# Kernel tuning notes

Measured on AMD Instinct MI355X. Metric: run time of the kernel, lower is better.

## Reference

```python
import jax, jax.numpy as jnp
import numpy as np

N_NODES = 50000
N_EDGES = 800000
N_GRAPHS = 512
EPS = 1e-5
SLOPE = 0.2  # LeakyReLU negative slope in GATv2


def setup_inputs() -> dict:
    key = jax.random.key(0)
    ks = jax.random.split(key, 20)
    s = 0.1
    inp = {
        "x": jax.random.normal(ks[0], (N_NODES, 9), jnp.float32),
        "edge_attr": jax.random.normal(ks[1], (N_EDGES, 3), jnp.float32),
        "Wl0": jax.random.normal(ks[2], (9, 64), jnp.float32) * s,
        "Wr0": jax.random.normal(ks[3], (9, 64), jnp.float32) * s,
        "bl0": jnp.zeros((64,), jnp.float32),
        "br0": jnp.zeros((64,), jnp.float32),
        "We0": jax.random.normal(ks[4], (3, 64), jnp.float32) * s,
        "att0": jax.random.normal(ks[5], (64,), jnp.float32) * s,
        "bo0": jnp.zeros((64,), jnp.float32),
        "Wl": jax.random.normal(ks[6], (4, 64, 64), jnp.float32) * s,
        "Wr": jax.random.normal(ks[7], (4, 64, 64), jnp.float32) * s,
        "bl": jnp.zeros((4, 64), jnp.float32),
        "br": jnp.zeros((4, 64), jnp.float32),
        "We": jax.random.normal(ks[8], (4, 3, 64), jnp.float32) * s,
        "att": jax.random.normal(ks[9], (4, 64), jnp.float32) * s,
        "bo": jnp.zeros((4, 64), jnp.float32),
        "bn_g": jnp.ones((5, 64), jnp.float32),
        "bn_b": jnp.zeros((5, 64), jnp.float32),
        "bn_m": jnp.zeros((5, 64), jnp.float32),
        "bn_v": jax.random.uniform(ks[10], (5, 64), jnp.float32, 0.5, 1.5),
        "Wjk": jax.random.normal(ks[11], (64, 64), jnp.float32) * s,
        "bjk": jnp.zeros((64,), jnp.float32),
        "Whead": jax.random.normal(ks[12], (64, 1), jnp.float32) * s,
        "bhead": jnp.zeros((1,), jnp.float32),
        "edge_index": jax.random.randint(ks[13], (2, N_EDGES), 0, N_NODES, jnp.int32),
        "batch": jnp.sort(jax.random.randint(ks[14], (N_NODES,), 0, N_GRAPHS, jnp.int32)),
        "num_graphs": N_GRAPHS,
    }
    return inp


def gatv2_layer(h, src, dst, ea, Wl_, bl_, Wr_, br_, We_, a_, bo_, n_nodes):
    # GATv2Conv (heads=1, edge_dim) : e_ij = a . LeakyReLU(Wl h_j + Wr h_i + We e_ij)
    xl = h @ Wl_ + bl_                          # [N, 64] source transform
    xr = h @ Wr_ + br_                          # [N, 64] dest transform
    e = jax.nn.leaky_relu(xl[src] + xr[dst] + ea @ We_, SLOPE)  # [E, 64]
    logit = e @ a_                              # [E]
    m = jax.ops.segment_max(logit, dst, num_segments=n_nodes)
    m = jnp.where(jnp.isfinite(m), m, 0.0)      # empty segments -> -inf
    p = jnp.exp(logit - m[dst])
    z = jax.ops.segment_sum(p, dst, num_segments=n_nodes)
    alpha = p / jnp.maximum(z[dst], 1e-16)      # softmax over in-edges of dst
    out = jax.ops.segment_sum(alpha[:, None] * xl[src], dst, num_segments=n_nodes)
    return out + bo_


def bn_relu(h, g, b, m, v):
    # eval-mode BatchNorm1d followed by ReLU (BasicGNN: norm then act)
    return jax.nn.relu((h - m) * (g * jax.lax.rsqrt(v + EPS)) + b)


def reference(x, edge_attr, Wl0, Wr0, bl0, br0, We0, att0, bo0,
              Wl, Wr, bl, br, We, att, bo,
              bn_g, bn_b, bn_m, bn_v, Wjk, bjk, Whead, bhead,
              edge_index, batch, num_graphs):
    n = x.shape[0]
    src, dst = edge_index[0], edge_index[1]
    h = gatv2_layer(x, src, dst, edge_attr, Wl0, bl0, Wr0, br0, We0, att0, bo0, n)
    h = bn_relu(h, bn_g[0], bn_b[0], bn_m[0], bn_v[0])
    for i in range(4):
        h = gatv2_layer(h, src, dst, edge_attr, Wl[i], bl[i], Wr[i], br[i], We[i], att[i], bo[i], n)
        h = bn_relu(h, bn_g[i + 1], bn_b[i + 1], bn_m[i + 1], bn_v[i + 1])
    h = h @ Wjk + bjk                            # jk='last' output projection 64->64
    # global mean pool over graphs
    sums = jax.ops.segment_sum(h, batch, num_segments=num_graphs)          # [G, 64]
    cnt = jax.ops.segment_sum(jnp.ones((n,), h.dtype), batch, num_segments=num_graphs)
    pooled = sums / jnp.maximum(cnt, 1.0)[:, None]
    return pooled @ Whead + bhead                # [G, 1]  (dropout inactive in eval)
```

## Files before the change

kernel.cpp:

```cpp
#include <hip/hip_runtime.h>
#include <math.h>

#define N_NODES 50000
#define N_EDGES 800000
#define N_GRAPHS 512
#define SLOPE 0.2f
#define CAP 48
static constexpr float EPS_BN = 1e-5f;

typedef float v2f __attribute__((ext_vector_type(2)));


__global__ void scatter_bucket_kernel(const int* __restrict__ src, const int* __restrict__ dst,
                                      const float* __restrict__ ea,
                                      int* __restrict__ cnt,
                                      float4* __restrict__ rec) {
    int e = blockIdx.x * blockDim.x + threadIdx.x;
    if (e < N_EDGES) {
        int d = dst[e];
        int pos = atomicAdd(&cnt[d], 1);
        if (pos < CAP)
            rec[(size_t)d * CAP + pos] = make_float4(__int_as_float(src[e]),
                                                     ea[e * 3 + 0], ea[e * 3 + 1], ea[e * 3 + 2]);
    }
}


__global__ __launch_bounds__(256) void transform9_kernel(
    const float* __restrict__ h,
    const float* __restrict__ Wl, const float* __restrict__ bl,
    const float* __restrict__ Wr, const float* __restrict__ br,
    float* __restrict__ xl, float* __restrict__ xr) {
    int t = threadIdx.x;
    int w = t >> 6;
    int k = t & 63;
    v2f wlr[9];
#pragma unroll
    for (int j = 0; j < 9; j++) wlr[j] = (v2f){Wl[j * 64 + k], Wr[j * 64 + k]};
    v2f bias = {bl[k], br[k]};
    int wid = blockIdx.x * 4 + w;
    const int NW = gridDim.x * 4;
    for (int n = wid; n < N_NODES; n += NW) {
        int un = __builtin_amdgcn_readfirstlane(n);
        const float* __restrict__ hrow = h + (size_t)un * 9;
        float hb[9];
#pragma unroll
        for (int j = 0; j < 9; j++) hb[j] = hrow[j];
        v2f acc = bias;
#pragma unroll
        for (int j = 0; j < 9; j++)
            acc = __builtin_elementwise_fma((v2f){hb[j], hb[j]}, wlr[j], acc);
        xl[(size_t)un * 64 + k] = acc.x;
        xr[(size_t)un * 64 + k] = acc.y;
    }
}


__global__ __launch_bounds__(256) void transform5_kernel(
    const float* __restrict__ h,
    const float* __restrict__ Wl, const float* __restrict__ bl,
    const float* __restrict__ Wr, const float* __restrict__ br,
    float* __restrict__ xl, float* __restrict__ xr) {
    __shared__ float sAt[64][68];
    __shared__ float sB[64][128];
    int t = threadIdx.x;
    int n0 = blockIdx.x * 64;

#pragma unroll
    for (int i = 0; i < 4; i++) {
        int idx = i * 256 + t;
        int row = idx >> 4;
        int fc  = idx & 15;
        int n = n0 + row;
        float4 v = (n < N_NODES) ? *((const float4*)(h + (size_t)n * 64 + fc * 4))
                                 : make_float4(0.f, 0.f, 0.f, 0.f);
        sAt[fc * 4 + 0][row] = v.x;
        sAt[fc * 4 + 1][row] = v.y;
        sAt[fc * 4 + 2][row] = v.z;
        sAt[fc * 4 + 3][row] = v.w;
    }
#pragma unroll
    for (int i = 0; i < 8; i++) {
        int idx = i * 256 + t;
        int j  = idx >> 5;
        int fc = idx & 31;
        int c  = fc * 4;
        float4 v = (c < 64) ? *((const float4*)(Wl + j * 64 + c))
                            : *((const float4*)(Wr + j * 64 + (c - 64)));
        *((float4*)&sB[j][c]) = v;
    }
    __syncthreads();

    int tx = t & 15, ty = t >> 4;
    int col0 = tx * 8;
    const float* bsrc = (col0 < 64) ? (bl + col0) : (br + (col0 - 64));
    v2f acc[4][4];
#pragma unroll
    for (int r = 0; r < 4; r++)
#pragma unroll
        for (int cc = 0; cc < 4; cc++)
            acc[r][cc] = (v2f){bsrc[cc * 2], bsrc[cc * 2 + 1]};

#pragma unroll 4
    for (int j = 0; j < 64; j++) {
        float a0 = sAt[j][ty * 4 + 0];
        float a1 = sAt[j][ty * 4 + 1];
        float a2 = sAt[j][ty * 4 + 2];
        float a3 = sAt[j][ty * 4 + 3];
        float4 bq0 = *((const float4*)&sB[j][col0]);
        float4 bq1 = *((const float4*)&sB[j][col0 + 4]);
        v2f b0 = {bq0.x, bq0.y}, b1 = {bq0.z, bq0.w};
        v2f b2 = {bq1.x, bq1.y}, b3 = {bq1.z, bq1.w};
        v2f a0v = {a0, a0}, a1v = {a1, a1}, a2v = {a2, a2}, a3v = {a3, a3};
        acc[0][0] = __builtin_elementwise_fma(a0v, b0, acc[0][0]);
        acc[0][1] = __builtin_elementwise_fma(a0v, b1, acc[0][1]);
        acc[0][2] = __builtin_elementwise_fma(a0v, b2, acc[0][2]);
        acc[0][3] = __builtin_elementwise_fma(a0v, b3, acc[0][3]);
        acc[1][0] = __builtin_elementwise_fma(a1v, b0, acc[1][0]);
        acc[1][1] = __builtin_elementwise_fma(a1v, b1, acc[1][1]);
        acc[1][2] = __builtin_elementwise_fma(a1v, b2, acc[1][2]);
        acc[1][3] = __builtin_elementwise_fma(a1v, b3, acc[1][3]);
        acc[2][0] = __builtin_elementwise_fma(a2v, b0, acc[2][0]);
        acc[2][1] = __builtin_elementwise_fma(a2v, b1, acc[2][1]);
        acc[2][2] = __builtin_elementwise_fma(a2v, b2, acc[2][2]);
        acc[2][3] = __builtin_elementwise_fma(a2v, b3, acc[2][3]);
        acc[3][0] = __builtin_elementwise_fma(a3v, b0, acc[3][0]);
        acc[3][1] = __builtin_elementwise_fma(a3v, b1, acc[3][1]);
        acc[3][2] = __builtin_elementwise_fma(a3v, b2, acc[3][2]);
        acc[3][3] = __builtin_elementwise_fma(a3v, b3, acc[3][3]);
    }

#pragma unroll
    for (int r = 0; r < 4; r++) {
        int n = n0 + ty * 4 + r;
        if (n < N_NODES) {
            float4 lo = make_float4(acc[r][0].x, acc[r][0].y, acc[r][1].x, acc[r][1].y);
            float4 hi = make_float4(acc[r][2].x, acc[r][2].y, acc[r][3].x, acc[r][3].y);
            float* dst = (col0 < 64) ? (xl + (size_t)n * 64 + col0)
                                     : (xr + (size_t)n * 64 + (col0 - 64));
            *((float4*)dst) = lo;
            *((float4*)(dst + 4)) = hi;
        }
    }
}


__global__ __launch_bounds__(256) void gat_fused4_kernel(
    const float* __restrict__ xl, const float* __restrict__ xr,
    const float4* __restrict__ recP, const int* __restrict__ cnt,
    const float* __restrict__ We, const float* __restrict__ att,
    const float* __restrict__ bo,
    const float* __restrict__ bn_g, const float* __restrict__ bn_b,
    const float* __restrict__ bn_m, const float* __restrict__ bn_v,
    float* __restrict__ hout) {
    int t = threadIdx.x;
    int w = t >> 6;
    int lane = t & 63;
    int q = lane >> 4;
    int r = lane & 15;
    int k4 = r * 4;
    int n = blockIdx.x * 4 + w;

    float4 we0 = *(const float4*)(We + 0 * 64 + k4);
    float4 we1 = *(const float4*)(We + 64 + k4);
    float4 we2 = *(const float4*)(We + 128 + k4);
    float4 at4 = *(const float4*)(att + k4);
    float4 xq  = *(const float4*)(xr + (size_t)n * 64 + k4);
    v2f we0a = {we0.x, we0.y}, we0b = {we0.z, we0.w};
    v2f we1a = {we1.x, we1.y}, we1b = {we1.z, we1.w};
    v2f we2a = {we2.x, we2.y}, we2b = {we2.z, we2.w};
    v2f ata  = {at4.x, at4.y}, atb  = {at4.z, at4.w};
    v2f xra  = {xq.x, xq.y},   xrb  = {xq.z, xq.w};
    int beg = n * CAP;
    int end = beg + min(cnt[n], CAP);

    v2f oAa = {0.f, 0.f}, oAb = {0.f, 0.f};
    v2f oBa = {0.f, 0.f}, oBb = {0.f, 0.f};
    float zA = 0.f, zB = 0.f;

    for (int c = beg; c < end; c += 8) {
        int pA = c + q;     bool vA = pA < end; int iA = vA ? pA : beg;
        int pB = c + 4 + q; bool vB = pB < end; int iB = vB ? pB : beg;
        float4 rA = recP[iA];
        float4 rB = recP[iB];
        int sA = __float_as_int(rA.x);
        int sB = __float_as_int(rB.x);
        float4 xA = *(const float4*)(xl + (size_t)sA * 64 + k4);
        float4 xB = *(const float4*)(xl + (size_t)sB * 64 + k4);
        v2f xAa = {xA.x, xA.y}, xAb = {xA.z, xA.w};
        v2f xBa = {xB.x, xB.y}, xBb = {xB.z, xB.w};

        v2f tAa = xAa + xra, tAb = xAb + xrb;
        v2f tBa = xBa + xra, tBb = xBb + xrb;
        tAa = __builtin_elementwise_fma((v2f){rA.y, rA.y}, we0a, tAa);
        tAb = __builtin_elementwise_fma((v2f){rA.y, rA.y}, we0b, tAb);
        tBa = __builtin_elementwise_fma((v2f){rB.y, rB.y}, we0a, tBa);
        tBb = __builtin_elementwise_fma((v2f){rB.y, rB.y}, we0b, tBb);
        tAa = __builtin_elementwise_fma((v2f){rA.z, rA.z}, we1a, tAa);
        tAb = __builtin_elementwise_fma((v2f){rA.z, rA.z}, we1b, tAb);
        tBa = __builtin_elementwise_fma((v2f){rB.z, rB.z}, we1a, tBa);
        tBb = __builtin_elementwise_fma((v2f){rB.z, rB.z}, we1b, tBb);
        tAa = __builtin_elementwise_fma((v2f){rA.w, rA.w}, we2a, tAa);
        tAb = __builtin_elementwise_fma((v2f){rA.w, rA.w}, we2b, tAb);
        tBa = __builtin_elementwise_fma((v2f){rB.w, rB.w}, we2a, tBa);
        tBb = __builtin_elementwise_fma((v2f){rB.w, rB.w}, we2b, tBb);

        tAa = __builtin_elementwise_max(tAa, tAa * SLOPE);
        tAb = __builtin_elementwise_max(tAb, tAb * SLOPE);
        tBa = __builtin_elementwise_max(tBa, tBa * SLOPE);
        tBb = __builtin_elementwise_max(tBb, tBb * SLOPE);

        v2f dA = ata * tAa; dA = __builtin_elementwise_fma(atb, tAb, dA);
        v2f dB = ata * tBa; dB = __builtin_elementwise_fma(atb, tBb, dB);
        float accA = dA.x + dA.y;
        float accB = dB.x + dB.y;

        accA += __shfl_xor(accA, 1, 64);  accB += __shfl_xor(accB, 1, 64);
        accA += __shfl_xor(accA, 2, 64);  accB += __shfl_xor(accB, 2, 64);
        accA += __shfl_xor(accA, 4, 64);  accB += __shfl_xor(accB, 4, 64);
        accA += __shfl_xor(accA, 8, 64);  accB += __shfl_xor(accB, 8, 64);

        float peA = vA ? __expf(accA) : 0.f;
        float peB = vB ? __expf(accB) : 0.f;
        v2f pA2 = {peA, peA}, pB2 = {peB, peB};
        oAa = __builtin_elementwise_fma(pA2, xAa, oAa);
        oAb = __builtin_elementwise_fma(pA2, xAb, oAb);
        oBa = __builtin_elementwise_fma(pB2, xBa, oBa);
        oBb = __builtin_elementwise_fma(pB2, xBb, oBb);
        zA += peA; zB += peB;
    }

    v2f oa = oAa + oBa, ob = oAb + oBb;
    float z = zA + zB;
    float4 o = make_float4(oa.x, oa.y, ob.x, ob.y);
    o.x += __shfl_xor(o.x, 16, 64); o.x += __shfl_xor(o.x, 32, 64);
    o.y += __shfl_xor(o.y, 16, 64); o.y += __shfl_xor(o.y, 32, 64);
    o.z += __shfl_xor(o.z, 16, 64); o.z += __shfl_xor(o.z, 32, 64);
    o.w += __shfl_xor(o.w, 16, 64); o.w += __shfl_xor(o.w, 32, 64);
    z += __shfl_xor(z, 16, 64); z += __shfl_xor(z, 32, 64);

    if (q == 0) {
        float zi = 1.0f / fmaxf(z, 1e-16f);
        float4 bo4 = *(const float4*)(bo + k4);
        float4 g4  = *(const float4*)(bn_g + k4);
        float4 b4  = *(const float4*)(bn_b + k4);
        float4 m4  = *(const float4*)(bn_m + k4);
        float4 v4  = *(const float4*)(bn_v + k4);
        float4 res;
        res.x = fmaxf((o.x * zi + bo4.x - m4.x) * (g4.x / sqrtf(v4.x + EPS_BN)) + b4.x, 0.f);
        res.y = fmaxf((o.y * zi + bo4.y - m4.y) * (g4.y / sqrtf(v4.y + EPS_BN)) + b4.y, 0.f);
        res.z = fmaxf((o.z * zi + bo4.z - m4.z) * (g4.z / sqrtf(v4.z + EPS_BN)) + b4.z, 0.f);
        res.w = fmaxf((o.w * zi + bo4.w - m4.w) * (g4.w / sqrtf(v4.w + EPS_BN)) + b4.w, 0.f);
        *(float4*)(hout + (size_t)n * 64 + k4) = res;
    }
}


__global__ __launch_bounds__(64) void pool_all_kernel(
    const float* __restrict__ h, const int* __restrict__ batch,
    const float* __restrict__ Wjk, const float* __restrict__ bjk,
    const float* __restrict__ Whead, const float* __restrict__ bhead,
    float* __restrict__ out) {
    int g = blockIdx.x;
    int k = threadIdx.x;
    int lo = 0, hi = N_NODES;
    while (lo < hi) { int mid = (lo + hi) >> 1; if (batch[mid] < g) lo = mid + 1; else hi = mid; }
    int s = lo;
    hi = N_NODES;
    while (lo < hi) { int mid = (lo + hi) >> 1; if (batch[mid] < g + 1) lo = mid + 1; else hi = mid; }
    int e = lo;

    float wc = 0.f;
    for (int j = 0; j < 64; j++) wc = fmaf(Wjk[k * 64 + j], Whead[j], wc);
    float bc = bjk[k] * Whead[k];
    for (int off = 32; off > 0; off >>= 1) bc += __shfl_xor(bc, off, 64);

    float acc = 0.f;
    for (int n = s; n < e; ++n) acc += h[(size_t)n * 64 + k];
    float cntf = (float)(e - s);
    acc /= fmaxf(cntf, 1.0f);
    float v = acc * wc;
    for (int off = 32; off > 0; off >>= 1) v += __shfl_xor(v, off, 64);
    if (k == 0) out[g] = v + bc + bhead[0];
}


extern "C" void kernel_launch(void* const* d_in, const int* in_sizes, int n_in,
                              void* d_out, int out_size, void* d_ws, size_t ws_size,
                              hipStream_t stream) {
    const float* x     = (const float*)d_in[0];
    const float* ea    = (const float*)d_in[1];
    const float* Wl0   = (const float*)d_in[2];
    const float* Wr0   = (const float*)d_in[3];
    const float* bl0   = (const float*)d_in[4];
    const float* br0   = (const float*)d_in[5];
    const float* We0   = (const float*)d_in[6];
    const float* att0  = (const float*)d_in[7];
    const float* bo0   = (const float*)d_in[8];
    const float* Wl    = (const float*)d_in[9];
    const float* Wr    = (const float*)d_in[10];
    const float* bl    = (const float*)d_in[11];
    const float* br    = (const float*)d_in[12];
    const float* We    = (const float*)d_in[13];
    const float* att   = (const float*)d_in[14];
    const float* bo    = (const float*)d_in[15];
    const float* bn_g  = (const float*)d_in[16];
    const float* bn_b  = (const float*)d_in[17];
    const float* bn_m  = (const float*)d_in[18];
    const float* bn_v  = (const float*)d_in[19];
    const float* Wjk   = (const float*)d_in[20];
    const float* bjk   = (const float*)d_in[21];
    const float* Whead = (const float*)d_in[22];
    const float* bhead = (const float*)d_in[23];
    const int* edge_index = (const int*)d_in[24];
    const int* batch      = (const int*)d_in[25];

    const int* srcIdx = edge_index;
    const int* dstIdx = edge_index + N_EDGES;

    char* ws = (char*)d_ws;
    size_t off = 0;
    auto alloc = [&](size_t bytes) -> void* {
        void* p = ws + off;
        off += (bytes + 255) & ~(size_t)255;
        return p;
    };
    float* hA      = (float*)alloc((size_t)N_NODES * 64 * 4);
    float* hB      = (float*)alloc((size_t)N_NODES * 64 * 4);
    float* xlb     = (float*)alloc((size_t)N_NODES * 64 * 4);
    float* xrb     = (float*)alloc((size_t)N_NODES * 64 * 4);
    int*   cnt     = (int*)alloc((size_t)N_NODES * 4);
    float4* recP   = (float4*)alloc((size_t)N_NODES * CAP * 16);

    hipMemsetAsync(cnt, 0, (size_t)N_NODES * 4, stream);
    scatter_bucket_kernel<<<(N_EDGES + 255) / 256, 256, 0, stream>>>(srcIdx, dstIdx, ea,
                                                                     cnt, recP);

    const int NBN = N_NODES / 4;
    const int NBG = (N_NODES + 63) / 64;

    transform9_kernel<<<512, 256, 0, stream>>>(x, Wl0, bl0, Wr0, br0, xlb, xrb);
    gat_fused4_kernel<<<NBN, 256, 0, stream>>>(xlb, xrb, recP, cnt,
                                               We0, att0, bo0,
                                               bn_g, bn_b, bn_m, bn_v, hA);

    float* hcur = hA;
    float* hnext = hB;
    for (int i = 0; i < 4; i++) {
        transform5_kernel<<<NBG, 256, 0, stream>>>(hcur,
            Wl + (size_t)i * 64 * 64, bl + (size_t)i * 64,
            Wr + (size_t)i * 64 * 64, br + (size_t)i * 64,
            xlb, xrb);
        gat_fused4_kernel<<<NBN, 256, 0, stream>>>(xlb, xrb, recP, cnt,
            We + (size_t)i * 3 * 64, att + (size_t)i * 64,
            bo + (size_t)i * 64,
            bn_g + (size_t)(i + 1) * 64, bn_b + (size_t)(i + 1) * 64,
            bn_m + (size_t)(i + 1) * 64, bn_v + (size_t)(i + 1) * 64,
            hnext);
        float* tp = hcur; hcur = hnext; hnext = tp;
    }

    pool_all_kernel<<<N_GRAPHS, 64, 0, stream>>>(hcur, batch, Wjk, bjk, Whead, bhead,
                                                 (float*)d_out);
}
```

Baseline: 503.5 us.

## Fuse all GNN layers into one persistent cooperative kernel with grid syncs

Replaces the chain of separate scatter, transform, GAT and pool launches with a single persistent cooperative kernel. Phases are separated by grid-wide barriers and work is distributed with grid-stride loops. The aim is to remove per-launch overhead and inter-kernel gaps. In exchange, occupancy is capped by the persistent grid size and launch bounds, and each grid.sync adds its own barrier cost. The scatter and transform9 phases now run concurrently before the first barrier, which is safe because they touch disjoint data.

```diff
diff --git a/kernel.cpp b/kernel.cpp
--- a/kernel.cpp
+++ b/kernel.cpp
@@ -1,151 +1,159 @@
 #include <hip/hip_runtime.h>
+#include <hip/hip_cooperative_groups.h>
 #include <math.h>
+
+namespace cg = cooperative_groups;
 
 #define N_NODES 50000
 #define N_EDGES 800000
 #define N_GRAPHS 512
 #define SLOPE 0.2f
 #define CAP 48
+#define NQUADS 12500
+#define NTILES 782
 static constexpr float EPS_BN = 1e-5f;
 
 typedef float v2f __attribute__((ext_vector_type(2)));
 
-
-__global__ void scatter_bucket_kernel(const int* __restrict__ src, const int* __restrict__ dst,
-                                      const float* __restrict__ ea,
-                                      int* __restrict__ cnt,
-                                      float4* __restrict__ rec) {
-    int e = blockIdx.x * blockDim.x + threadIdx.x;
-    if (e < N_EDGES) {
-        int d = dst[e];
-        int pos = atomicAdd(&cnt[d], 1);
+struct MegaParams {
+    const float *x, *ea;
+    const float *Wl0, *Wr0, *bl0, *br0, *We0, *att0, *bo0;
+    const float *Wl, *Wr, *bl, *br, *We, *att, *bo;
+    const float *bn_g, *bn_b, *bn_m, *bn_v;
+    const float *Wjk, *bjk, *Whead, *bhead;
+    const int *src, *dst, *batch;
+    float *hA, *hB, *xl, *xr;
+    int *cnt;
+    float4 *rec;
+    float *out;
+};
+
+__device__ __forceinline__ void scatter_phase(const MegaParams& p, int nthreads) {
+    int gtid = blockIdx.x * 256 + threadIdx.x;
+    for (int e = gtid; e < N_EDGES; e += nthreads) {
+        int d = p.dst[e];
+        int pos = atomicAdd(&p.cnt[d], 1);
         if (pos < CAP)
-            rec[(size_t)d * CAP + pos] = make_float4(__int_as_float(src[e]),
-                                                     ea[e * 3 + 0], ea[e * 3 + 1], ea[e * 3 + 2]);
-    }
-}
-
-
-__global__ __launch_bounds__(256) void transform9_kernel(
+            p.rec[(size_t)d * CAP + pos] =
+                make_float4(__int_as_float(p.src[e]),
+                            p.ea[e * 3 + 0], p.ea[e * 3 + 1], p.ea[e * 3 + 2]);
+    }
+}
+
+__device__ __forceinline__ void transform9_phase(const MegaParams& p) {
+    int t = threadIdx.x;
+    int w = t >> 6;
+    int k = t & 63;
+    v2f wlr[9];
+#pragma unroll
+    for (int j = 0; j < 9; j++) wlr[j] = (v2f){p.Wl0[j * 64 + k], p.Wr0[j * 64 + k]};
+    v2f bias = {p.bl0[k], p.br0[k]};
+    const int NW = gridDim.x * 4;
+    for (int n = blockIdx.x * 4 + w; n < N_NODES; n += NW) {
+        int un = __builtin_amdgcn_readfirstlane(n);
+        const float* __restrict__ hrow = p.x + (size_t)un * 9;
+        float hb[9];
+#pragma unroll
+        for (int j = 0; j < 9; j++) hb[j] = hrow[j];
+        v2f acc = bias;
+#pragma unroll
+        for (int j = 0; j < 9; j++)
+            acc = __builtin_elementwise_fma((v2f){hb[j], hb[j]}, wlr[j], acc);
+        p.xl[(size_t)un * 64 + k] = acc.x;
+        p.xr[(size_t)un * 64 + k] = acc.y;
+    }
+}
+
+__device__ __forceinline__ void transform64_phase(
+    float sAt[64][68], float sB[64][128],
     const float* __restrict__ h,
     const float* __restrict__ Wl, const float* __restrict__ bl,
     const float* __restrict__ Wr, const float* __restrict__ br,
     float* __restrict__ xl, float* __restrict__ xr) {
     int t = threadIdx.x;
-    int w = t >> 6;
-    int k = t & 63;
-    v2f wlr[9];
-#pragma unroll
-    for (int j = 0; j < 9; j++) wlr[j] = (v2f){Wl[j * 64 + k], Wr[j * 64 + k]};
-    v2f bias = {bl[k], br[k]};
-    int wid = blockIdx.x * 4 + w;
-    const int NW = gridDim.x * 4;
-    for (int n = wid; n < N_NODES; n += NW) {
-        int un = __builtin_amdgcn_readfirstlane(n);
-        const float* __restrict__ hrow = h + (size_t)un * 9;
-        float hb[9];
-#pragma unroll
-        for (int j = 0; j < 9; j++) hb[j] = hrow[j];
-        v2f acc = bias;
-#pragma unroll
-        for (int j = 0; j < 9; j++)
-            acc = __builtin_elementwise_fma((v2f){hb[j], hb[j]}, wlr[j], acc);
-        xl[(size_t)un * 64 + k] = acc.x;
-        xr[(size_t)un * 64 + k] = acc.y;
-    }
-}
-
-
-__global__ __launch_bounds__(256) void transform5_kernel(
-    const float* __restrict__ h,
-    const float* __restrict__ Wl, const float* __restrict__ bl,
-    const float* __restrict__ Wr, const float* __restrict__ br,
-    float* __restrict__ xl, float* __restrict__ xr) {
-    __shared__ float sAt[64][68];
-    __shared__ float sB[64][128];
-    int t = threadIdx.x;
-    int n0 = blockIdx.x * 64;
-
-#pragma unroll
-    for (int i = 0; i < 4; i++) {
-        int idx = i * 256 + t;
-        int row = idx >> 4;
-        int fc  = idx & 15;
-        int n = n0 + row;
-        float4 v = (n < N_NODES) ? *((const float4*)(h + (size_t)n * 64 + fc * 4))
-                                 : make_float4(0.f, 0.f, 0.f, 0.f);
-        sAt[fc * 4 + 0][row] = v.x;
-        sAt[fc * 4 + 1][row] = v.y;
-        sAt[fc * 4 + 2][row] = v.z;
-        sAt[fc * 4 + 3][row] = v.w;
-    }
-#pragma unroll
-    for (int i = 0; i < 8; i++) {
-        int idx = i * 256 + t;
-        int j  = idx >> 5;
-        int fc = idx & 31;
-        int c  = fc * 4;
-        float4 v = (c < 64) ? *((const float4*)(Wl + j * 64 + c))
-                            : *((const float4*)(Wr + j * 64 + (c - 64)));
-        *((float4*)&sB[j][c]) = v;
-    }
-    __syncthreads();
-
-    int tx = t & 15, ty = t >> 4;
-    int col0 = tx * 8;
-    const float* bsrc = (col0 < 64) ? (bl + col0) : (br + (col0 - 64));
-    v2f acc[4][4];
-#pragma unroll
-    for (int r = 0; r < 4; r++)
-#pragma unroll
-        for (int cc = 0; cc < 4; cc++)
-            acc[r][cc] = (v2f){bsrc[cc * 2], bsrc[cc * 2 + 1]};
+    for (int tile = blockIdx.x; tile < NTILES; tile += gridDim.x) {
+        int n0 = tile * 64;
+#pragma unroll
+        for (int i = 0; i < 4; i++) {
+            int idx = i * 256 + t;
+            int row = idx >> 4;
+            int fc  = idx & 15;
+            int n = n0 + row;
+            float4 v = (n < N_NODES) ? *((const float4*)(h + (size_t)n * 64 + fc * 4))
+                                     : make_float4(0.f, 0.f, 0.f, 0.f);
+            sAt[fc * 4 + 0][row] = v.x;
+            sAt[fc * 4 + 1][row] = v.y;
+            sAt[fc * 4 + 2][row] = v.z;
+            sAt[fc * 4 + 3][row] = v.w;
+        }
+#pragma unroll
+        for (int i = 0; i < 8; i++) {
+            int idx = i * 256 + t;
+            int j  = idx >> 5;
+            int fc = idx & 31;
+            int c  = fc * 4;
+            float4 v = (c < 64) ? *((const float4*)(Wl + j * 64 + c))
+                                : *((const float4*)(Wr + j * 64 + (c - 64)));
+            *((float4*)&sB[j][c]) = v;
+        }
+        __syncthreads();
+
+        int tx = t & 15, ty = t >> 4;
+        int col0 = tx * 8;
+        const float* bsrc = (col0 < 64) ? (bl + col0) : (br + (col0 - 64));
+        v2f acc[4][4];
+#pragma unroll
+        for (int r = 0; r < 4; r++)
+#pragma unroll
+            for (int cc = 0; cc < 4; cc++)
+                acc[r][cc] = (v2f){bsrc[cc * 2], bsrc[cc * 2 + 1]};
 
 #pragma unroll 4
-    for (int j = 0; j < 64; j++) {
-        float a0 = sAt[j][ty * 4 + 0];
-        float a1 = sAt[j][ty * 4 + 1];
-        float a2 = sAt[j][ty * 4 + 2];
-        float a3 = sAt[j][ty * 4 + 3];
-        float4 bq0 = *((const float4*)&sB[j][col0]);
-        float4 bq1 = *((const float4*)&sB[j][col0 + 4]);
-        v2f b0 = {bq0.x, bq0.y}, b1 = {bq0.z, bq0.w};
-        v2f b2 = {bq1.x, bq1.y}, b3 = {bq1.z, bq1.w};
-        v2f a0v = {a0, a0}, a1v = {a1, a1}, a2v = {a2, a2}, a3v = {a3, a3};
-        acc[0][0] = __builtin_elementwise_fma(a0v, b0, acc[0][0]);
-        acc[0][1] = __builtin_elementwise_fma(a0v, b1, acc[0][1]);
-        acc[0][2] = __builtin_elementwise_fma(a0v, b2, acc[0][2]);
-        acc[0][3] = __builtin_elementwise_fma(a0v, b3, acc[0][3]);
-        acc[1][0] = __builtin_elementwise_fma(a1v, b0, acc[1][0]);
-        acc[1][1] = __builtin_elementwise_fma(a1v, b1, acc[1][1]);
-        acc[1][2] = __builtin_elementwise_fma(a1v, b2, acc[1][2]);
-        acc[1][3] = __builtin_elementwise_fma(a1v, b3, acc[1][3]);
-        acc[2][0] = __builtin_elementwise_fma(a2v, b0, acc[2][0]);
-        acc[2][1] = __builtin_elementwise_fma(a2v, b1, acc[2][1]);
-        acc[2][2] = __builtin_elementwise_fma(a2v, b2, acc[2][2]);
-        acc[2][3] = __builtin_elementwise_fma(a2v, b3, acc[2][3]);
-        acc[3][0] = __builtin_elementwise_fma(a3v, b0, acc[3][0]);
-        acc[3][1] = __builtin_elementwise_fma(a3v, b1, acc[3][1]);
-        acc[3][2] = __builtin_elementwise_fma(a3v, b2, acc[3][2]);
-        acc[3][3] = __builtin_elementwise_fma(a3v, b3, acc[3][3]);
-    }
-
-#pragma unroll
-    for (int r = 0; r < 4; r++) {
-        int n = n0 + ty * 4 + r;
-        if (n < N_NODES) {
-            float4 lo = make_float4(acc[r][0].x, acc[r][0].y, acc[r][1].x, acc[r][1].y);
-            float4 hi = make_float4(acc[r][2].x, acc[r][2].y, acc[r][3].x, acc[r][3].y);
-            float* dst = (col0 < 64) ? (xl + (size_t)n * 64 + col0)
-                                     : (xr + (size_t)n * 64 + (col0 - 64));
-            *((float4*)dst) = lo;
-            *((float4*)(dst + 4)) = hi;
-        }
-    }
-}
-
-
-__global__ __launch_bounds__(256) void gat_fused4_kernel(
+        for (int j = 0; j < 64; j++) {
+            float a0 = sAt[j][ty * 4 + 0];
+            float a1 = sAt[j][ty * 4 + 1];
+            float a2 = sAt[j][ty * 4 + 2];
+            float a3 = sAt[j][ty * 4 + 3];
+            float4 bq0 = *((const float4*)&sB[j][col0]);
+            float4 bq1 = *((const float4*)&sB[j][col0 + 4]);
+            v2f b0 = {bq0.x, bq0.y}, b1 = {bq0.z, bq0.w};
+            v2f b2 = {bq1.x, bq1.y}, b3 = {bq1.z, bq1.w};
+            v2f a0v = {a0, a0}, a1v = {a1, a1}, a2v = {a2, a2}, a3v = {a3, a3};
+            acc[0][0] = __builtin_elementwise_fma(a0v, b0, acc[0][0]);
+            acc[0][1] = __builtin_elementwise_fma(a0v, b1, acc[0][1]);
+            acc[0][2] = __builtin_elementwise_fma(a0v, b2, acc[0][2]);
+            acc[0][3] = __builtin_elementwise_fma(a0v, b3, acc[0][3]);
+            acc[1][0] = __builtin_elementwise_fma(a1v, b0, acc[1][0]);
+            acc[1][1] = __builtin_elementwise_fma(a1v, b1, acc[1][1]);
+            acc[1][2] = __builtin_elementwise_fma(a1v, b2, acc[1][2]);
+            acc[1][3] = __builtin_elementwise_fma(a1v, b3, acc[1][3]);
+            acc[2][0] = __builtin_elementwise_fma(a2v, b0, acc[2][0]);
+            acc[2][1] = __builtin_elementwise_fma(a2v, b1, acc[2][1]);
+            acc[2][2] = __builtin_elementwise_fma(a2v, b2, acc[2][2]);
+            acc[2][3] = __builtin_elementwise_fma(a2v, b3, acc[2][3]);
+            acc[3][0] = __builtin_elementwise_fma(a3v, b0, acc[3][0]);
+            acc[3][1] = __builtin_elementwise_fma(a3v, b1, acc[3][1]);
+            acc[3][2] = __builtin_elementwise_fma(a3v, b2, acc[3][2]);
+            acc[3][3] = __builtin_elementwise_fma(a3v, b3, acc[3][3]);
+        }
+
+#pragma unroll
+        for (int r = 0; r < 4; r++) {
+            int n = n0 + ty * 4 + r;
+            if (n < N_NODES) {
+                float4 lo = make_float4(acc[r][0].x, acc[r][0].y, acc[r][1].x, acc[r][1].y);
+                float4 hi = make_float4(acc[r][2].x, acc[r][2].y, acc[r][3].x, acc[r][3].y);
+                float* dstp = (col0 < 64) ? (xl + (size_t)n * 64 + col0)
+                                          : (xr + (size_t)n * 64 + (col0 - 64));
+                *((float4*)dstp) = lo;
+                *((float4*)(dstp + 4)) = hi;
+            }
+        }
+        __syncthreads();
+    }
+}
+
+__device__ __forceinline__ void gat_phase(
     const float* __restrict__ xl, const float* __restrict__ xr,
     const float4* __restrict__ recP, const int* __restrict__ cnt,
     const float* __restrict__ We, const float* __restrict__ att,
@@ -159,207 +167,226 @@
     int q = lane >> 4;
     int r = lane & 15;
     int k4 = r * 4;
-    int n = blockIdx.x * 4 + w;
 
     float4 we0 = *(const float4*)(We + 0 * 64 + k4);
     float4 we1 = *(const float4*)(We + 64 + k4);
     float4 we2 = *(const float4*)(We + 128 + k4);
     float4 at4 = *(const float4*)(att + k4);
-    float4 xq  = *(const float4*)(xr + (size_t)n * 64 + k4);
     v2f we0a = {we0.x, we0.y}, we0b = {we0.z, we0.w};
     v2f we1a = {we1.x, we1.y}, we1b = {we1.z, we1.w};
     v2f we2a = {we2.x, we2.y}, we2b = {we2.z, we2.w};
     v2f ata  = {at4.x, at4.y}, atb  = {at4.z, at4.w};
-    v2f xra  = {xq.x, xq.y},   xrb  = {xq.z, xq.w};
-    int beg = n * CAP;
-    int end = beg + min(cnt[n], CAP);
-
-    v2f oAa = {0.f, 0.f}, oAb = {0.f, 0.f};
-    v2f oBa = {0.f, 0.f}, oBb = {0.f, 0.f};
-    float zA = 0.f, zB = 0.f;
-
-    for (int c = beg; c < end; c += 8) {
-        int pA = c + q;     bool vA = pA < end; int iA = vA ? pA : beg;
-        int pB = c + 4 + q; bool vB = pB < end; int iB = vB ? pB : beg;
-        float4 rA = recP[iA];
-        float4 rB = recP[iB];
-        int sA = __float_as_int(rA.x);
-        int sB = __float_as_int(rB.x);
-        float4 xA = *(const float4*)(xl + (size_t)sA * 64 + k4);
-        float4 xB = *(const float4*)(xl + (size_t)sB * 64 + k4);
-        v2f xAa = {xA.x, xA.y}, xAb = {xA.z, xA.w};
-        v2f xBa = {xB.x, xB.y}, xBb = {xB.z, xB.w};
-
-        v2f tAa = xAa + xra, tAb = xAb + xrb;
-        v2f tBa = xBa + xra, tBb = xBb + xrb;
-        tAa = __builtin_elementwise_fma((v2f){rA.y, rA.y}, we0a, tAa);
-        tAb = __builtin_elementwise_fma((v2f){rA.y, rA.y}, we0b, tAb);
-        tBa = __builtin_elementwise_fma((v2f){rB.y, rB.y}, we0a, tBa);
-        tBb = __builtin_elementwise_fma((v2f){rB.y, rB.y}, we0b, tBb);
-        tAa = __builtin_elementwise_fma((v2f){rA.z, rA.z}, we1a, tAa);
-        tAb = __builtin_elementwise_fma((v2f){rA.z, rA.z}, we1b, tAb);
-        tBa = __builtin_elementwise_fma((v2f){rB.z, rB.z}, we1a, tBa);
-        tBb = __builtin_elementwise_fma((v2f){rB.z, rB.z}, we1b, tBb);
-        tAa = __builtin_elementwise_fma((v2f){rA.w, rA.w}, we2a, tAa);
-        tAb = __builtin_elementwise_fma((v2f){rA.w, rA.w}, we2b, tAb);
-        tBa = __builtin_elementwise_fma((v2f){rB.w, rB.w}, we2a, tBa);
-        tBb = __builtin_elementwise_fma((v2f){rB.w, rB.w}, we2b, tBb);
-
-        tAa = __builtin_elementwise_max(tAa, tAa * SLOPE);
-        tAb = __builtin_elementwise_max(tAb, tAb * SLOPE);
-        tBa = __builtin_elementwise_max(tBa, tBa * SLOPE);
-        tBb = __builtin_elementwise_max(tBb, tBb * SLOPE);
-
-        v2f dA = ata * tAa; dA = __builtin_elementwise_fma(atb, tAb, dA);
-        v2f dB = ata * tBa; dB = __builtin_elementwise_fma(atb, tBb, dB);
-        float accA = dA.x + dA.y;
-        float accB = dB.x + dB.y;
-
-        accA += __shfl_xor(accA, 1, 64);  accB += __shfl_xor(accB, 1, 64);
-        accA += __shfl_xor(accA, 2, 64);  accB += __shfl_xor(accB, 2, 64);
-        accA += __shfl_xor(accA, 4, 64);  accB += __shfl_xor(accB, 4, 64);
-        accA += __shfl_xor(accA, 8, 64);  accB += __shfl_xor(accB, 8, 64);
-
-        float peA = vA ? __expf(accA) : 0.f;
-        float peB = vB ? __expf(accB) : 0.f;
-        v2f pA2 = {peA, peA}, pB2 = {peB, peB};
-        oAa = __builtin_elementwise_fma(pA2, xAa, oAa);
-        oAb = __builtin_elementwise_fma(pA2, xAb, oAb);
-        oBa = __builtin_elementwise_fma(pB2, xBa, oBa);
-        oBb = __builtin_elementwise_fma(pB2, xBb, oBb);
-        zA += peA; zB += peB;
-    }
-
-    v2f oa = oAa + oBa, ob = oAb + oBb;
-    float z = zA + zB;
-    float4 o = make_float4(oa.x, oa.y, ob.x, ob.y);
-    o.x += __shfl_xor(o.x, 16, 64); o.x += __shfl_xor(o.x, 32, 64);
-    o.y += __shfl_xor(o.y, 16, 64); o.y += __shfl_xor(o.y, 32, 64);
-    o.z += __shfl_xor(o.z, 16, 64); o.z += __shfl_xor(o.z, 32, 64);
-    o.w += __shfl_xor(o.w, 16, 64); o.w += __shfl_xor(o.w, 32, 64);
-    z += __shfl_xor(z, 16, 64); z += __shfl_xor(z, 32, 64);
-
-    if (q == 0) {
-        float zi = 1.0f / fmaxf(z, 1e-16f);
-        float4 bo4 = *(const float4*)(bo + k4);
-        float4 g4  = *(const float4*)(bn_g + k4);
-        float4 b4  = *(const float4*)(bn_b + k4);
-        float4 m4  = *(const float4*)(bn_m + k4);
-        float4 v4  = *(const float4*)(bn_v + k4);
-        float4 res;
-        res.x = fmaxf((o.x * zi + bo4.x - m4.x) * (g4.x / sqrtf(v4.x + EPS_BN)) + b4.x, 0.f);
-        res.y = fmaxf((o.y * zi + bo4.y - m4.y) * (g4.y / sqrtf(v4.y + EPS_BN)) + b4.y, 0.f);
-        res.z = fmaxf((o.z * zi + bo4.z - m4.z) * (g4.z / sqrtf(v4.z + EPS_BN)) + b4.z, 0.f);
-        res.w = fmaxf((o.w * zi + bo4.w - m4.w) * (g4.w / sqrtf(v4.w + EPS_BN)) + b4.w, 0.f);
-        *(float4*)(hout + (size_t)n * 64 + k4) = res;
-    }
-}
-
-
-__global__ __launch_bounds__(64) void pool_all_kernel(
-    const float* __restrict__ h, const int* __restrict__ batch,
-    const float* __restrict__ Wjk, const float* __restrict__ bjk,
-    const float* __restrict__ Whead, const float* __restrict__ bhead,
-    float* __restrict__ out) {
-    int g = blockIdx.x;
-    int k = threadIdx.x;
-    int lo = 0, hi = N_NODES;
-    while (lo < hi) { int mid = (lo + hi) >> 1; if (batch[mid] < g) lo = mid + 1; else hi = mid; }
-    int s = lo;
-    hi = N_NODES;
-    while (lo < hi) { int mid = (lo + hi) >> 1; if (batch[mid] < g + 1) lo = mid + 1; else hi = mid; }
-    int e = lo;
-
-    float wc = 0.f;
-    for (int j = 0; j < 64; j++) wc = fmaf(Wjk[k * 64 + j], Whead[j], wc);
-    float bc = bjk[k] * Whead[k];
-    for (int off = 32; off > 0; off >>= 1) bc += __shfl_xor(bc, off, 64);
-
-    float acc = 0.f;
-    for (int n = s; n < e; ++n) acc += h[(size_t)n * 64 + k];
-    float cntf = (float)(e - s);
-    acc /= fmaxf(cntf, 1.0f);
-    float v = acc * wc;
-    for (int off = 32; off > 0; off >>= 1) v += __shfl_xor(v, off, 64);
-    if (k == 0) out[g] = v + bc + bhead[0];
+    float4 bo4 = *(const float4*)(bo + k4);
+    float4 g4  = *(const float4*)(bn_g + k4);
+    float4 b4  = *(const float4*)(bn_b + k4);
+    float4 m4  = *(const float4*)(bn_m + k4);
+    float4 v4  = *(const float4*)(bn_v + k4);
+
+    for (int blk = blockIdx.x; blk < NQUADS; blk += gridDim.x) {
+        int n = blk * 4 + w;
+        float4 xq = *(const float4*)(xr + (size_t)n * 64 + k4);
+        v2f xra = {xq.x, xq.y}, xrb = {xq.z, xq.w};
+        int beg = n * CAP;
+        int end = beg + min(cnt[n], CAP);
+
+        v2f oAa = {0.f, 0.f}, oAb = {0.f, 0.f};
+        v2f oBa = {0.f, 0.f}, oBb = {0.f, 0.f};
+        float zA = 0.f, zB = 0.f;
+
+        for (int c = beg; c < end; c += 8) {
+            int pA = c + q;     bool vA = pA < end; int iA = vA ? pA : beg;
+            int pB = c + 4 + q; bool vB = pB < end; int iB = vB ? pB : beg;
+            float4 rA = recP[iA];
+            float4 rB = recP[iB];
+            int sA = __float_as_int(rA.x);
+            int sB = __float_as_int(rB.x);
+            float4 xA = *(const float4*)(xl + (size_t)sA * 64 + k4);
+            float4 xB = *(const float4*)(xl + (size_t)sB * 64 + k4);
+            v2f xAa = {xA.x, xA.y}, xAb = {xA.z, xA.w};
+            v2f xBa = {xB.x, xB.y}, xBb = {xB.z, xB.w};
+
+            v2f tAa = xAa + xra, tAb = xAb + xrb;
+            v2f tBa = xBa + xra, tBb = xBb + xrb;
+            tAa = __builtin_elementwise_fma((v2f){rA.y, rA.y}, we0a, tAa);
+            tAb = __builtin_elementwise_fma((v2f){rA.y, rA.y}, we0b, tAb);
+            tBa = __builtin_elementwise_fma((v2f){rB.y, rB.y}, we0a, tBa);
+            tBb = __builtin_elementwise_fma((v2f){rB.y, rB.y}, we0b, tBb);
+            tAa = __builtin_elementwise_fma((v2f){rA.z, rA.z}, we1a, tAa);
+            tAb = __builtin_elementwise_fma((v2f){rA.z, rA.z}, we1b, tAb);
+            tBa = __builtin_elementwise_fma((v2f){rB.z, rB.z}, we1a, tBa);
+            tBb = __builtin_elementwise_fma((v2f){rB.z, rB.z}, we1b, tBb);
+            tAa = __builtin_elementwise_fma((v2f){rA.w, rA.w}, we2a, tAa);
+            tAb = __builtin_elementwise_fma((v2f){rA.w, rA.w}, we2b, tAb);
+            tBa = __builtin_elementwise_fma((v2f){rB.w, rB.w}, we2a, tBa);
+            tBb = __builtin_elementwise_fma((v2f){rB.w, rB.w}, we2b, tBb);
+
+            tAa = __builtin_elementwise_max(tAa, tAa * SLOPE);
+            tAb = __builtin_elementwise_max(tAb, tAb * SLOPE);
+            tBa = __builtin_elementwise_max(tBa, tBa * SLOPE);
+            tBb = __builtin_elementwise_max(tBb, tBb * SLOPE);
+
+            v2f dA = ata * tAa; dA = __builtin_elementwise_fma(atb, tAb, dA);
+            v2f dB = ata * tBa; dB = __builtin_elementwise_fma(atb, tBb, dB);
+            float accA = dA.x + dA.y;
+            float accB = dB.x + dB.y;
+
+            accA += __shfl_xor(accA, 1, 64);  accB += __shfl_xor(accB, 1, 64);
+            accA += __shfl_xor(accA, 2, 64);  accB += __shfl_xor(accB, 2, 64);
+            accA += __shfl_xor(accA, 4, 64);  accB += __shfl_xor(accB, 4, 64);
+            accA += __shfl_xor(accA, 8, 64);  accB += __shfl_xor(accB, 8, 64);
+
+            float peA = vA ? __expf(accA) : 0.f;
+            float peB = vB ? __expf(accB) : 0.f;
+            v2f pA2 = {peA, peA}, pB2 = {peB, peB};
+            oAa = __builtin_elementwise_fma(pA2, xAa, oAa);
+            oAb = __builtin_elementwise_fma(pA2, xAb, oAb);
+            oBa = __builtin_elementwise_fma(pB2, xBa, oBa);
+            oBb = __builtin_elementwise_fma(pB2, xBb, oBb);
+            zA += peA; zB += peB;
+        }
+
+        v2f oa = oAa + oBa, ob = oAb + oBb;
+        float z = zA + zB;
+        float4 o = make_float4(oa.x, oa.y, ob.x, ob.y);
+        o.x += __shfl_xor(o.x, 16, 64); o.x += __shfl_xor(o.x, 32, 64);
+        o.y += __shfl_xor(o.y, 16, 64); o.y += __shfl_xor(o.y, 32, 64);
+        o.z += __shfl_xor(o.z, 16, 64); o.z += __shfl_xor(o.z, 32, 64);
+        o.w += __shfl_xor(o.w, 16, 64); o.w += __shfl_xor(o.w, 32, 64);
+        z += __shfl_xor(z, 16, 64); z += __shfl_xor(z, 32, 64);
+
+        if (q == 0) {
+            float zi = 1.0f / fmaxf(z, 1e-16f);
+            float4 res;
+            res.x = fmaxf((o.x * zi + bo4.x - m4.x) * (g4.x / sqrtf(v4.x + EPS_BN)) + b4.x, 0.f);
+            res.y = fmaxf((o.y * zi + bo4.y - m4.y) * (g4.y / sqrtf(v4.y + EPS_BN)) + b4.y, 0.f);
+            res.z = fmaxf((o.z * zi + bo4.z - m4.z) * (g4.z / sqrtf(v4.z + EPS_BN)) + b4.z, 0.f);
+            res.w = fmaxf((o.w * zi + bo4.w - m4.w) * (g4.w / sqrtf(v4.w + EPS_BN)) + b4.w, 0.f);
+            *(float4*)(hout + (size_t)n * 64 + k4) = res;
+        }
+    }
+}
+
+__device__ __forceinline__ void pool_phase(const MegaParams& p, const float* __restrict__ h) {
+    int t = threadIdx.x;
+    int w = t >> 6;
+    int k = t & 63;
+    for (int g = blockIdx.x * 4 + w; g < N_GRAPHS; g += gridDim.x * 4) {
+        int lo = 0, hi = N_NODES;
+        while (lo < hi) { int mid = (lo + hi) >> 1; if (p.batch[mid] < g) lo = mid + 1; else hi = mid; }
+        int s = lo;
+        hi = N_NODES;
+        while (lo < hi) { int mid = (lo + hi) >> 1; if (p.batch[mid] < g + 1) lo = mid + 1; else hi = mid; }
+        int e = lo;
+
+        float wc = 0.f;
+        for (int j = 0; j < 64; j++) wc = fmaf(p.Wjk[k * 64 + j], p.Whead[j], wc);
+        float bc = p.bjk[k] * p.Whead[k];
+        for (int off = 32; off > 0; off >>= 1) bc += __shfl_xor(bc, off, 64);
+
+        float acc = 0.f;
+        for (int n = s; n < e; ++n) acc += h[(size_t)n * 64 + k];
+        float cntf = (float)(e - s);
+        acc /= fmaxf(cntf, 1.0f);
+        float v = acc * wc;
+        for (int off = 32; off > 0; off >>= 1) v += __shfl_xor(v, off, 64);
+        if (k == 0) p.out[g] = v + bc + p.bhead[0];
+    }
+}
+
+
+__global__ __launch_bounds__(256, 3) void mega_kernel(MegaParams p) {
+    __shared__ float sAt[64][68];
+    __shared__ float sB[64][128];
+    cg::grid_group grid = cg::this_grid();
+    int nthreads = gridDim.x * 256;
+
+    scatter_phase(p, nthreads);
+    transform9_phase(p);
+    grid.sync();
+
+    gat_phase(p.xl, p.xr, p.rec, p.cnt, p.We0, p.att0, p.bo0,
+              p.bn_g, p.bn_b, p.bn_m, p.bn_v, p.hA);
+    grid.sync();
+
+    float* hcur = p.hA;
+    float* hnext = p.hB;
+    for (int i = 0; i < 4; i++) {
+        transform64_phase(sAt, sB, hcur,
+                          p.Wl + (size_t)i * 64 * 64, p.bl + (size_t)i * 64,
+                          p.Wr + (size_t)i * 64 * 64, p.br + (size_t)i * 64,
+                          p.xl, p.xr);
+        grid.sync();
+        gat_phase(p.xl, p.xr, p.rec, p.cnt,
+                  p.We + (size_t)i * 3 * 64, p.att + (size_t)i * 64,
+                  p.bo + (size_t)i * 64,
+                  p.bn_g + (size_t)(i + 1) * 64, p.bn_b + (size_t)(i + 1) * 64,
+                  p.bn_m + (size_t)(i + 1) * 64, p.bn_v + (size_t)(i + 1) * 64,
+                  hnext);
+        grid.sync();
+        float* tp = hcur; hcur = hnext; hnext = tp;
+    }
+
+    pool_phase(p, hcur);
 }
 
 
 extern "C" void kernel_launch(void* const* d_in, const int* in_sizes, int n_in,
                               void* d_out, int out_size, void* d_ws, size_t ws_size,
                               hipStream_t stream) {
-    const float* x     = (const float*)d_in[0];
-    const float* ea    = (const float*)d_in[1];
-    const float* Wl0   = (const float*)d_in[2];
-    const float* Wr0   = (const float*)d_in[3];
-    const float* bl0   = (const float*)d_in[4];
-    const float* br0   = (const float*)d_in[5];
-    const float* We0   = (const float*)d_in[6];
-    const float* att0  = (const float*)d_in[7];
-    const float* bo0   = (const float*)d_in[8];
-    const float* Wl    = (const float*)d_in[9];
-    const float* Wr    = (const float*)d_in[10];
-    const float* bl    = (const float*)d_in[11];
-    const float* br    = (const float*)d_in[12];
-    const float* We    = (const float*)d_in[13];
-    const float* att   = (const float*)d_in[14];
-    const float* bo    = (const float*)d_in[15];
-    const float* bn_g  = (const float*)d_in[16];
-    const float* bn_b  = (const float*)d_in[17];
-    const float* bn_m  = (const float*)d_in[18];
-    const float* bn_v  = (const float*)d_in[19];
-    const float* Wjk   = (const float*)d_in[20];
-    const float* bjk   = (const float*)d_in[21];
-    const float* Whead = (const float*)d_in[22];
-    const float* bhead = (const float*)d_in[23];
+    MegaParams p;
+    p.x     = (const float*)d_in[0];
+    p.ea    = (const float*)d_in[1];
+    p.Wl0   = (const float*)d_in[2];
+    p.Wr0   = (const float*)d_in[3];
+    p.bl0   = (const float*)d_in[4];
+    p.br0   = (const float*)d_in[5];
+    p.We0   = (const float*)d_in[6];
+    p.att0  = (const float*)d_in[7];
+    p.bo0   = (const float*)d_in[8];
+    p.Wl    = (const float*)d_in[9];
+    p.Wr    = (const float*)d_in[10];
+    p.bl    = (const float*)d_in[11];
+    p.br    = (const float*)d_in[12];
+    p.We    = (const float*)d_in[13];
+    p.att   = (const float*)d_in[14];
+    p.bo    = (const float*)d_in[15];
+    p.bn_g  = (const float*)d_in[16];
+    p.bn_b  = (const float*)d_in[17];
+    p.bn_m  = (const float*)d_in[18];
+    p.bn_v  = (const float*)d_in[19];
+    p.Wjk   = (const float*)d_in[20];
+    p.bjk   = (const float*)d_in[21];
+    p.Whead = (const float*)d_in[22];
+    p.bhead = (const float*)d_in[23];
     const int* edge_index = (const int*)d_in[24];
-    const int* batch      = (const int*)d_in[25];
-
-    const int* srcIdx = edge_index;
-    const int* dstIdx = edge_index + N_EDGES;
+    p.batch = (const int*)d_in[25];
+    p.src = edge_index;
+    p.dst = edge_index + N_EDGES;
+    p.out = (float*)d_out;
 
     char* ws = (char*)d_ws;
     size_t off = 0;
     auto alloc = [&](size_t bytes) -> void* {
-        void* p = ws + off;
+        void* q = ws + off;
         off += (bytes + 255) & ~(size_t)255;
-        return p;
+        return q;
     };
-    float* hA      = (float*)alloc((size_t)N_NODES * 64 * 4);
-    float* hB      = (float*)alloc((size_t)N_NODES * 64 * 4);
-    float* xlb     = (float*)alloc((size_t)N_NODES * 64 * 4);
-    float* xrb     = (float*)alloc((size_t)N_NODES * 64 * 4);
-    int*   cnt     = (int*)alloc((size_t)N_NODES * 4);
-    float4* recP   = (float4*)alloc((size_t)N_NODES * CAP * 16);
-
-    hipMemsetAsync(cnt, 0, (size_t)N_NODES * 4, stream);
-    scatter_bucket_kernel<<<(N_EDGES + 255) / 256, 256, 0, stream>>>(srcIdx, dstIdx, ea,
-                                                                     cnt, recP);
-
-    const int NBN = N_NODES / 4;
-    const int NBG = (N_NODES + 63) / 64;
-
-    transform9_kernel<<<512, 256, 0, stream>>>(x, Wl0, bl0, Wr0, br0, xlb, xrb);
-    gat_fused4_kernel<<<NBN, 256, 0, stream>>>(xlb, xrb, recP, cnt,
-                                               We0, att0, bo0,
-                                               bn_g, bn_b, bn_m, bn_v, hA);
-
-    float* hcur = hA;
-    float* hnext = hB;
-    for (int i = 0; i < 4; i++) {
-        transform5_kernel<<<NBG, 256, 0, stream>>>(hcur,
-            Wl + (size_t)i * 64 * 64, bl + (size_t)i * 64,
-            Wr + (size_t)i * 64 * 64, br + (size_t)i * 64,
-            xlb, xrb);
-        gat_fused4_kernel<<<NBN, 256, 0, stream>>>(xlb, xrb, recP, cnt,
-            We + (size_t)i * 3 * 64, att + (size_t)i * 64,
-            bo + (size_t)i * 64,
-            bn_g + (size_t)(i + 1) * 64, bn_b + (size_t)(i + 1) * 64,
-            bn_m + (size_t)(i + 1) * 64, bn_v + (size_t)(i + 1) * 64,
-            hnext);
-        float* tp = hcur; hcur = hnext; hnext = tp;
-    }
-
-    pool_all_kernel<<<N_GRAPHS, 64, 0, stream>>>(hcur, batch, Wjk, bjk, Whead, bhead,
-                                                 (float*)d_out);
-}
+    p.hA  = (float*)alloc((size_t)N_NODES * 64 * 4);
+    p.hB  = (float*)alloc((size_t)N_NODES * 64 * 4);
+    p.xl  = (float*)alloc((size_t)N_NODES * 64 * 4);
+    p.xr  = (float*)alloc((size_t)N_NODES * 64 * 4);
+    p.cnt = (int*)alloc((size_t)N_NODES * 4);
+    p.rec = (float4*)alloc((size_t)N_NODES * CAP * 16);
+
+    hipMemsetAsync(p.cnt, 0, (size_t)N_NODES * 4, stream);
+
+    int maxPerCU = 0;
+    hipOccupancyMaxActiveBlocksPerMultiprocessor(&maxPerCU, mega_kernel, 256, 0);
+    if (maxPerCU < 1) maxPerCU = 1;
+    int grid = maxPerCU * 256;
+    if (grid > 768) grid = 768;
+
+    void* kargs[] = { (void*)&p };
+    hipLaunchCooperativeKernel((const void*)mega_kernel, dim3(grid), dim3(256),
+                               kargs, 0, stream);
+}
```

Result: slower. 1.318 ms (+161.8%).

## Fuse scatter with first transform and store compact edge buckets with indirect attribute loads

Applied to the files above, without the earlier changes.

Merges the edge bucketing kernel with the first-layer 9->64 node transform into one launch. Bucket records shrink from float4 (src plus three edge attributes) to int2 (src, edge id), and each GAT layer now gathers the three edge attributes from the original edge array through the edge id. This halves bucket storage and scatter write traffic, and removes one launch. In exchange it adds a dependent, scattered load of edge attributes in each of the five attention layers.

```diff
diff --git a/kernel.cpp b/kernel.cpp
--- a/kernel.cpp
+++ b/kernel.cpp
@@ -11,38 +11,31 @@
 typedef float v2f __attribute__((ext_vector_type(2)));
 
 
-__global__ void scatter_bucket_kernel(const int* __restrict__ src, const int* __restrict__ dst,
-                                      const float* __restrict__ ea,
-                                      int* __restrict__ cnt,
-                                      float4* __restrict__ rec) {
-    int e = blockIdx.x * blockDim.x + threadIdx.x;
+__global__ __launch_bounds__(256) void scatter_t9_kernel(
+    const int* __restrict__ src, const int* __restrict__ dst,
+    int* __restrict__ cnt, int2* __restrict__ bkt,
+    const float* __restrict__ x,
+    const float* __restrict__ Wl0, const float* __restrict__ bl0,
+    const float* __restrict__ Wr0, const float* __restrict__ br0,
+    float* __restrict__ xl, float* __restrict__ xr) {
+    int t = threadIdx.x;
+    int e = blockIdx.x * 256 + t;
     if (e < N_EDGES) {
         int d = dst[e];
         int pos = atomicAdd(&cnt[d], 1);
-        if (pos < CAP)
-            rec[(size_t)d * CAP + pos] = make_float4(__int_as_float(src[e]),
-                                                     ea[e * 3 + 0], ea[e * 3 + 1], ea[e * 3 + 2]);
-    }
-}
-
-
-__global__ __launch_bounds__(256) void transform9_kernel(
-    const float* __restrict__ h,
-    const float* __restrict__ Wl, const float* __restrict__ bl,
-    const float* __restrict__ Wr, const float* __restrict__ br,
-    float* __restrict__ xl, float* __restrict__ xr) {
-    int t = threadIdx.x;
+        if (pos < CAP) bkt[(size_t)d * CAP + pos] = make_int2(src[e], e);
+    }
+
     int w = t >> 6;
     int k = t & 63;
     v2f wlr[9];
 #pragma unroll
-    for (int j = 0; j < 9; j++) wlr[j] = (v2f){Wl[j * 64 + k], Wr[j * 64 + k]};
-    v2f bias = {bl[k], br[k]};
-    int wid = blockIdx.x * 4 + w;
+    for (int j = 0; j < 9; j++) wlr[j] = (v2f){Wl0[j * 64 + k], Wr0[j * 64 + k]};
+    v2f bias = {bl0[k], br0[k]};
     const int NW = gridDim.x * 4;
-    for (int n = wid; n < N_NODES; n += NW) {
+    for (int n = blockIdx.x * 4 + w; n < N_NODES; n += NW) {
         int un = __builtin_amdgcn_readfirstlane(n);
-        const float* __restrict__ hrow = h + (size_t)un * 9;
+        const float* __restrict__ hrow = x + (size_t)un * 9;
         float hb[9];
 #pragma unroll
         for (int j = 0; j < 9; j++) hb[j] = hrow[j];
@@ -136,18 +129,19 @@
         if (n < N_NODES) {
             float4 lo = make_float4(acc[r][0].x, acc[r][0].y, acc[r][1].x, acc[r][1].y);
             float4 hi = make_float4(acc[r][2].x, acc[r][2].y, acc[r][3].x, acc[r][3].y);
-            float* dst = (col0 < 64) ? (xl + (size_t)n * 64 + col0)
-                                     : (xr + (size_t)n * 64 + (col0 - 64));
-            *((float4*)dst) = lo;
-            *((float4*)(dst + 4)) = hi;
+            float* dstp = (col0 < 64) ? (xl + (size_t)n * 64 + col0)
+                                      : (xr + (size_t)n * 64 + (col0 - 64));
+            *((float4*)dstp) = lo;
+            *((float4*)(dstp + 4)) = hi;
         }
     }
 }
 
 
-__global__ __launch_bounds__(256) void gat_fused4_kernel(
+__global__ __launch_bounds__(256) void gat_fused6_kernel(
     const float* __restrict__ xl, const float* __restrict__ xr,
-    const float4* __restrict__ recP, const int* __restrict__ cnt,
+    const float* __restrict__ ea,
+    const int2* __restrict__ bkt, const int* __restrict__ cnt,
     const float* __restrict__ We, const float* __restrict__ att,
     const float* __restrict__ bo,
     const float* __restrict__ bn_g, const float* __restrict__ bn_b,
@@ -181,10 +175,14 @@
     for (int c = beg; c < end; c += 8) {
         int pA = c + q;     bool vA = pA < end; int iA = vA ? pA : beg;
         int pB = c + 4 + q; bool vB = pB < end; int iB = vB ? pB : beg;
-        float4 rA = recP[iA];
-        float4 rB = recP[iB];
-        int sA = __float_as_int(rA.x);
-        int sB = __float_as_int(rB.x);
+        int2 bA = bkt[iA];
+        int2 bB = bkt[iB];
+        int sA = bA.x, eA = bA.y;
+        int sB = bB.x, eB = bB.y;
+        const float* __restrict__ eaA = ea + (size_t)eA * 3;
+        const float* __restrict__ eaB = ea + (size_t)eB * 3;
+        float a_e0 = eaA[0], a_e1 = eaA[1], a_e2 = eaA[2];
+        float b_e0 = eaB[0], b_e1 = eaB[1], b_e2 = eaB[2];
         float4 xA = *(const float4*)(xl + (size_t)sA * 64 + k4);
         float4 xB = *(const float4*)(xl + (size_t)sB * 64 + k4);
         v2f xAa = {xA.x, xA.y}, xAb = {xA.z, xA.w};
@@ -192,18 +190,18 @@
 
         v2f tAa = xAa + xra, tAb = xAb + xrb;
         v2f tBa = xBa + xra, tBb = xBb + xrb;
-        tAa = __builtin_elementwise_fma((v2f){rA.y, rA.y}, we0a, tAa);
-        tAb = __builtin_elementwise_fma((v2f){rA.y, rA.y}, we0b, tAb);
-        tBa = __builtin_elementwise_fma((v2f){rB.y, rB.y}, we0a, tBa);
-        tBb = __builtin_elementwise_fma((v2f){rB.y, rB.y}, we0b, tBb);
-        tAa = __builtin_elementwise_fma((v2f){rA.z, rA.z}, we1a, tAa);
-        tAb = __builtin_elementwise_fma((v2f){rA.z, rA.z}, we1b, tAb);
-        tBa = __builtin_elementwise_fma((v2f){rB.z, rB.z}, we1a, tBa);
-        tBb = __builtin_elementwise_fma((v2f){rB.z, rB.z}, we1b, tBb);
-        tAa = __builtin_elementwise_fma((v2f){rA.w, rA.w}, we2a, tAa);
-        tAb = __builtin_elementwise_fma((v2f){rA.w, rA.w}, we2b, tAb);
-        tBa = __builtin_elementwise_fma((v2f){rB.w, rB.w}, we2a, tBa);
-        tBb = __builtin_elementwise_fma((v2f){rB.w, rB.w}, we2b, tBb);
+        tAa = __builtin_elementwise_fma((v2f){a_e0, a_e0}, we0a, tAa);
+        tAb = __builtin_elementwise_fma((v2f){a_e0, a_e0}, we0b, tAb);
+        tBa = __builtin_elementwise_fma((v2f){b_e0, b_e0}, we0a, tBa);
+        tBb = __builtin_elementwise_fma((v2f){b_e0, b_e0}, we0b, tBb);
+        tAa = __builtin_elementwise_fma((v2f){a_e1, a_e1}, we1a, tAa);
+        tAb = __builtin_elementwise_fma((v2f){a_e1, a_e1}, we1b, tAb);
+        tBa = __builtin_elementwise_fma((v2f){b_e1, b_e1}, we1a, tBa);
+        tBb = __builtin_elementwise_fma((v2f){b_e1, b_e1}, we1b, tBb);
+        tAa = __builtin_elementwise_fma((v2f){a_e2, a_e2}, we2a, tAa);
+        tAb = __builtin_elementwise_fma((v2f){a_e2, a_e2}, we2b, tAb);
+        tBa = __builtin_elementwise_fma((v2f){b_e2, b_e2}, we2a, tBa);
+        tBb = __builtin_elementwise_fma((v2f){b_e2, b_e2}, we2b, tBb);
 
         tAa = __builtin_elementwise_max(tAa, tAa * SLOPE);
         tAb = __builtin_elementwise_max(tAb, tAb * SLOPE);
@@ -330,17 +328,16 @@
     float* xlb     = (float*)alloc((size_t)N_NODES * 64 * 4);
     float* xrb     = (float*)alloc((size_t)N_NODES * 64 * 4);
     int*   cnt     = (int*)alloc((size_t)N_NODES * 4);
-    float4* recP   = (float4*)alloc((size_t)N_NODES * CAP * 16);
+    int2*  bkt     = (int2*)alloc((size_t)N_NODES * CAP * 8);
 
     hipMemsetAsync(cnt, 0, (size_t)N_NODES * 4, stream);
-    scatter_bucket_kernel<<<(N_EDGES + 255) / 256, 256, 0, stream>>>(srcIdx, dstIdx, ea,
-                                                                     cnt, recP);
+    scatter_t9_kernel<<<(N_EDGES + 255) / 256, 256, 0, stream>>>(
+        srcIdx, dstIdx, cnt, bkt, x, Wl0, bl0, Wr0, br0, xlb, xrb);
 
     const int NBN = N_NODES / 4;
     const int NBG = (N_NODES + 63) / 64;
 
-    transform9_kernel<<<512, 256, 0, stream>>>(x, Wl0, bl0, Wr0, br0, xlb, xrb);
-    gat_fused4_kernel<<<NBN, 256, 0, stream>>>(xlb, xrb, recP, cnt,
+    gat_fused6_kernel<<<NBN, 256, 0, stream>>>(xlb, xrb, ea, bkt, cnt,
                                                We0, att0, bo0,
                                                bn_g, bn_b, bn_m, bn_v, hA);
 
@@ -351,7 +348,7 @@
             Wl + (size_t)i * 64 * 64, bl + (size_t)i * 64,
             Wr + (size_t)i * 64 * 64, br + (size_t)i * 64,
             xlb, xrb);
-        gat_fused4_kernel<<<NBN, 256, 0, stream>>>(xlb, xrb, recP, cnt,
+        gat_fused6_kernel<<<NBN, 256, 0, stream>>>(xlb, xrb, ea, bkt, cnt,
             We + (size_t)i * 3 * 64, att + (size_t)i * 64,
             bo + (size_t)i * 64,
             bn_g + (size_t)(i + 1) * 64, bn_b + (size_t)(i + 1) * 64,
```

Result: slower. 523.8 us (+4.0%).
